# Optimization experiments

Hardware: AMD Instinct MI355X
Metric: run time of the kernel (lower is better)

The kernel has to match this reference:

```python
import jax, jax.numpy as jnp
import numpy as np

N = 50000
E = 800000
IN_DIM = 16
OUT_DIM = 16
EDGE_IN = 16
HID = 32


def setup_inputs() -> dict:
    key = jax.random.key(0)
    ks = jax.random.split(key, 9)
    x = jax.random.normal(ks[0], (N, IN_DIM), dtype=jnp.float32)
    edge_index = jax.random.randint(ks[1], (2, E), 0, N, dtype=jnp.int64)
    edge_attr = jax.random.normal(ks[2], (E, EDGE_IN), dtype=jnp.float32)
    # edge MLP params: Linear(EDGE_IN, 32) -> ReLU -> Linear(32, IN*OUT)
    w1 = jax.random.normal(ks[3], (EDGE_IN, HID), dtype=jnp.float32) * (1.0 / np.sqrt(EDGE_IN))
    b1 = jnp.zeros((HID,), dtype=jnp.float32)
    w2 = jax.random.normal(ks[4], (HID, IN_DIM * OUT_DIM), dtype=jnp.float32) * (1.0 / np.sqrt(HID))
    b2 = jnp.zeros((IN_DIM * OUT_DIM,), dtype=jnp.float32)
    # NNConv root weight and bias (defaults root_weight=True, bias=True)
    root = jax.random.normal(ks[5], (IN_DIM, OUT_DIM), dtype=jnp.float32) * (1.0 / np.sqrt(IN_DIM))
    bias = jnp.zeros((OUT_DIM,), dtype=jnp.float32)
    return {"x": x, "edge_index": edge_index, "edge_attr": edge_attr,
            "w1": w1, "b1": b1, "w2": w2, "b2": b2, "root": root, "bias": bias}


def reference(x, edge_index, edge_attr, w1, b1, w2, b2, root, bias):
    src = edge_index[0]  # x_j gathered from source nodes
    dst = edge_index[1]  # scatter-mean into target nodes
    # edge MLP -> per-edge weight matrix [E, IN, OUT]
    h = jax.nn.relu(edge_attr @ w1 + b1)
    W = (h @ w2 + b2).reshape(-1, IN_DIM, OUT_DIM)
    # per-edge matvec: message_e = x[src_e] @ W_e  -> [E, OUT]
    msg = jnp.einsum('ei,eio->eo', x[src], W)
    # scatter-mean aggregate into N target nodes
    summed = jax.ops.segment_sum(msg, dst, num_segments=N)
    cnt = jax.ops.segment_sum(jnp.ones((msg.shape[0],), dtype=msg.dtype), dst, num_segments=N)
    aggr = summed / jnp.maximum(cnt, 1.0)[:, None]
    return aggr + x @ root + bias
```

## Files before the change

kernel.cpp:

```cpp
#include <hip/hip_runtime.h>
#include <hip/hip_bf16.h>
#include <hip/hip_fp16.h>


#define N_NODES 50000
#define N_EDGES 800000
#define IN_D    16
#define OUT_D   16
#define HID_D   32
#define KTILES  17
#define NBLK_G  (N_NODES * OUT_D / 256)
#define EDGE_TPB   512
#define NBLK_E512  ((N_EDGES + EDGE_TPB - 1) / EDGE_TPB)
#define BLOB_BYTES 20480
#define BLOB_W1    17408
#define BLOB_B1    19456

typedef __attribute__((ext_vector_type(8))) _Float16 hfrag8;
typedef __attribute__((ext_vector_type(4))) float f32x4;

__device__ __forceinline__ void fma4(float a, const float4 w, float4& m) {
    m.x = fmaf(a, w.x, m.x);
    m.y = fmaf(a, w.y, m.y);
    m.z = fmaf(a, w.z, m.z);
    m.w = fmaf(a, w.w, m.w);
}
__device__ __forceinline__ int clampn(int v) {
    return v < 0 ? 0 : (v >= N_NODES ? N_NODES - 1 : v);
}
__device__ __forceinline__ void gload_lds16(const void* g, void* l) {
    __builtin_amdgcn_global_load_lds(
        (const __attribute__((address_space(1))) unsigned int*)g,
        (__attribute__((address_space(3))) unsigned int*)l,
        16, 0, 0);
}


__global__ __launch_bounds__(256) void setup_k(
    const float* __restrict__ w1,
    const float* __restrict__ b1,
    const float* __restrict__ w2,
    const float* __restrict__ b2,
    unsigned char* __restrict__ blob)
{
    const int t = threadIdx.x;
    __half* bp = reinterpret_cast<__half*>(blob);
    for (int r = t; r < KTILES * 32; r += 256) {
        const int tile = r >> 5, q = (r >> 3) & 3, j = r & 7;
        const int base = ((tile * 4 + q) * 16) * 8 + j;
        float vals[16];
        if (r < 512) {
            const float4* wr = reinterpret_cast<const float4*>(w2) + r * 4;
            float4 v0 = wr[0], v1 = wr[1], v2 = wr[2], v3 = wr[3];
            vals[0]=v0.x; vals[1]=v0.y; vals[2]=v0.z; vals[3]=v0.w;
            vals[4]=v1.x; vals[5]=v1.y; vals[6]=v1.z; vals[7]=v1.w;
            vals[8]=v2.x; vals[9]=v2.y; vals[10]=v2.z; vals[11]=v2.w;
            vals[12]=v3.x; vals[13]=v3.y; vals[14]=v3.z; vals[15]=v3.w;
        } else if (r < 528) {
            const float4* br = reinterpret_cast<const float4*>(b2) + (r - 512) * 4;
            float4 v0 = br[0], v1 = br[1], v2 = br[2], v3 = br[3];
            vals[0]=v0.x; vals[1]=v0.y; vals[2]=v0.z; vals[3]=v0.w;
            vals[4]=v1.x; vals[5]=v1.y; vals[6]=v1.z; vals[7]=v1.w;
            vals[8]=v2.x; vals[9]=v2.y; vals[10]=v2.z; vals[11]=v2.w;
            vals[12]=v3.x; vals[13]=v3.y; vals[14]=v3.z; vals[15]=v3.w;
        } else {
            #pragma unroll
            for (int o = 0; o < 16; ++o) vals[o] = 0.f;
        }
        #pragma unroll
        for (int o = 0; o < 16; ++o) bp[base + o * 8] = __float2half(vals[o]);
    }
    float* wf = reinterpret_cast<float*>(blob + BLOB_W1);
    wf[t] = w1[t];
    wf[t + 256] = w1[t + 256];
    if (t < HID_D) reinterpret_cast<float*>(blob + BLOB_B1)[t] = b1[t];
}


template <int MODE, int CAP>
__global__ __launch_bounds__(EDGE_TPB, 6) void edge_k(
    const float* __restrict__ x,
    const int*   __restrict__ ei,
    const float* __restrict__ ea,
    const unsigned char* __restrict__ gblob,
    int*   __restrict__ aux,
    int*   __restrict__ next,
    float* __restrict__ msg)
{
    __shared__ alignas(16) unsigned char s_blob[BLOB_BYTES];
    __shared__ alignas(16) __half s_h2[8 * 64 * 32];

    const int t    = threadIdx.x;
    const int lane = t & 63;
    const int w    = t >> 6;
    const int e    = blockIdx.x * EDGE_TPB + t;
    const bool wvalid = (blockIdx.x * EDGE_TPB + w * 64) < N_EDGES;

    #pragma unroll
    for (int j = 0; j < 3; ++j) {
        const int ch = w + 8 * j;
        if (ch < BLOB_BYTES / 1024)
            gload_lds16(gblob + ch * 1024 + lane * 16, s_blob + ch * 1024);
    }

    const hfrag8* s_B  = reinterpret_cast<const hfrag8*>(s_blob);
    const float4* s_w1 = reinterpret_cast<const float4*>(s_blob + BLOB_W1);
    const float4* s_b1 = reinterpret_cast<const float4*>(s_blob + BLOB_B1);

    const int q   = lane >> 4;
    const int n   = lane & 15;
    const int qh  = q >> 1;
    const int i0q = (q & 1) * 8;

    int slot = 0;
    float4 xpre[4][2];
    float eav[IN_D];

    if (wvalid) {
        const int src = clampn(ei[e]);
        const int dst = clampn(ei[N_EDGES + e]);
        if (MODE == 0) {
            int rank = atomicAdd(&aux[dst], 1);
            rank = rank < CAP ? rank : CAP - 1;
            slot = dst * CAP + rank;
        } else {
            next[e] = atomicExch(&aux[dst * 4 + (e & 3)], e);
            slot = e;
        }
        #pragma unroll
        for (int sub = 0; sub < 4; ++sub) {
            const int srcB = __shfl(src, sub * 16 + n, 64);
            const float4* xp = reinterpret_cast<const float4*>(x) + (size_t)srcB * 4 + (i0q >> 2);
            xpre[sub][0] = xp[0];
            xpre[sub][1] = xp[1];
        }
        const float4* eap = reinterpret_cast<const float4*>(ea) + (size_t)e * 4;
        float4 a0 = eap[0], a1 = eap[1], a2 = eap[2], a3 = eap[3];
        eav[0]=a0.x;  eav[1]=a0.y;  eav[2]=a0.z;  eav[3]=a0.w;
        eav[4]=a1.x;  eav[5]=a1.y;  eav[6]=a1.z;  eav[7]=a1.w;
        eav[8]=a2.x;  eav[9]=a2.y;  eav[10]=a2.z; eav[11]=a2.w;
        eav[12]=a3.x; eav[13]=a3.y; eav[14]=a3.z; eav[15]=a3.w;
    }

    __syncthreads();
    if (!wvalid) return;

    {
        float4 hv[HID_D / 4];
        #pragma unroll
        for (int j = 0; j < HID_D / 4; ++j) hv[j] = s_b1[j];
        #pragma unroll
        for (int i = 0; i < IN_D; ++i) {
            const float xi = eav[i];
            #pragma unroll
            for (int j = 0; j < HID_D / 4; ++j) fma4(xi, s_w1[i * (HID_D / 4) + j], hv[j]);
        }
        union { hfrag8 v[4]; __half h[32]; } hp;
        #pragma unroll
        for (int jj = 0; jj < 8; ++jj) {
            const int k0 = 4 * jj;
            hp.h[((k0 + 0) & 1) * 16 + ((k0 + 0) >> 1)] = __float2half(fmaxf(hv[jj].x, 0.f));
            hp.h[((k0 + 1) & 1) * 16 + ((k0 + 1) >> 1)] = __float2half(fmaxf(hv[jj].y, 0.f));
            hp.h[((k0 + 2) & 1) * 16 + ((k0 + 2) >> 1)] = __float2half(fmaxf(hv[jj].z, 0.f));
            hp.h[((k0 + 3) & 1) * 16 + ((k0 + 3) >> 1)] = __float2half(fmaxf(hv[jj].w, 0.f));
        }
        hfrag8* rowv = reinterpret_cast<hfrag8*>(s_h2 + (size_t)w * 2048 + lane * 32);
        const int swl = (lane >> 1) & 3;
        rowv[0 ^ swl] = hp.v[0];
        rowv[1 ^ swl] = hp.v[1];
        rowv[2 ^ swl] = hp.v[2];
        rowv[3 ^ swl] = hp.v[3];
    }
    asm volatile("s_waitcnt lgkmcnt(0)" ::: "memory");
    __builtin_amdgcn_wave_barrier();

    const __half* hbase = s_h2 + (size_t)w * 2048;
    #pragma unroll
    for (int sub = 0; sub < 4; ++sub) {
        const int posW = sub * 16 + n;
        __half2 xh[4];
        {
            float4 xa = xpre[sub][0], xb = xpre[sub][1];
            xh[0] = __float22half2_rn(make_float2(xa.x, xa.y));
            xh[1] = __float22half2_rn(make_float2(xa.z, xa.w));
            xh[2] = __float22half2_rn(make_float2(xb.x, xb.y));
            xh[3] = __float22half2_rn(make_float2(xb.z, xb.w));
        }
        union { hfrag8 v; __half h[8]; } hA, hB;
        {
            const hfrag8* rowv = reinterpret_cast<const hfrag8*>(hbase + posW * 32);
            const int swr = (posW >> 1) & 3;
            hA.v = rowv[(2 * qh + 0) ^ swr];
            hB.v = rowv[(2 * qh + 1) ^ swr];
        }
        f32x4 acc = {0.f, 0.f, 0.f, 0.f};
        #pragma unroll
        for (int tile = 0; tile < 16; ++tile) {
            const __half hs = (tile < 8) ? hA.h[tile] : hB.h[tile - 8];
            const __half2 hh = __half2half2(hs);
            union { hfrag8 v; __half2 h[4]; } a;
            a.h[0] = __hmul2(hh, xh[0]);
            a.h[1] = __hmul2(hh, xh[1]);
            a.h[2] = __hmul2(hh, xh[2]);
            a.h[3] = __hmul2(hh, xh[3]);
            acc = __builtin_amdgcn_mfma_f32_16x16x32_f16(a.v, s_B[tile * 64 + lane], acc, 0, 0, 0);
        }
        {
            union { hfrag8 v; __half2 h[4]; } a;
            if (qh == 0) { a.h[0]=xh[0]; a.h[1]=xh[1]; a.h[2]=xh[2]; a.h[3]=xh[3]; }
            else { hfrag8 z = {0,0,0,0,0,0,0,0}; a.v = z; }
            acc = __builtin_amdgcn_mfma_f32_16x16x32_f16(a.v, s_B[16 * 64 + lane], acc, 0, 0, 0);
        }
        #pragma unroll
        for (int r = 0; r < 4; ++r) {
            const int slotB = __shfl(slot, sub * 16 + q * 4 + r, 64);
            msg[(size_t)slotB * 16 + n] = acc[r];
        }
    }
}


template <int CAP>
__global__ __launch_bounds__(256) void gather_cap(
    const float* __restrict__ x,
    const float* __restrict__ root,
    const float* __restrict__ bias,
    const float* __restrict__ msg,
    const int*   __restrict__ cnt,
    float* __restrict__ out)
{
    __shared__ float4 s_root4[IN_D * 4];
    __shared__ float4 s_bias4[4];
    const int t = threadIdx.x;
    if (t < IN_D * 4) s_root4[t] = reinterpret_cast<const float4*>(root)[t];
    if (t < 4)        s_bias4[t] = reinterpret_cast<const float4*>(bias)[t];
    __syncthreads();

    const int g = blockIdx.x * 256 + t;
    const int n = g >> 4;
    const int l = t & 15;
    const int c = l >> 2;
    const int p = l & 3;

    const int d = cnt[n];
    const int m = d < CAP ? d : CAP;

    const float4* base = reinterpret_cast<const float4*>(msg) + (size_t)n * CAP * 4 + p;
    float4 a0 = make_float4(0.f, 0.f, 0.f, 0.f);
    float4 a1 = make_float4(0.f, 0.f, 0.f, 0.f);
    int j = c;
    for (; j + 4 < m; j += 8) {
        float4 v0 = base[(size_t)j * 4];
        float4 v1 = base[(size_t)(j + 4) * 4];
        a0.x += v0.x; a0.y += v0.y; a0.z += v0.z; a0.w += v0.w;
        a1.x += v1.x; a1.y += v1.y; a1.z += v1.z; a1.w += v1.w;
    }
    if (j < m) {
        float4 v0 = base[(size_t)j * 4];
        a0.x += v0.x; a0.y += v0.y; a0.z += v0.z; a0.w += v0.w;
    }
    float4 acc = make_float4(a0.x + a1.x, a0.y + a1.y, a0.z + a1.z, a0.w + a1.w);

    acc.x += __shfl_xor(acc.x, 4); acc.y += __shfl_xor(acc.y, 4);
    acc.z += __shfl_xor(acc.z, 4); acc.w += __shfl_xor(acc.w, 4);
    acc.x += __shfl_xor(acc.x, 8); acc.y += __shfl_xor(acc.y, 8);
    acc.z += __shfl_xor(acc.z, 8); acc.w += __shfl_xor(acc.w, 8);

    const float inv = 1.0f / (float)(d > 1 ? d : 1);
    float4 mv = s_bias4[p];
    mv.x += acc.x * inv; mv.y += acc.y * inv; mv.z += acc.z * inv; mv.w += acc.w * inv;

    {
        const float4* xp = reinterpret_cast<const float4*>(x) + (size_t)n * 4;
        float4 x0 = xp[0], x1 = xp[1], x2 = xp[2], x3 = xp[3];
        const float xs[IN_D] = { x0.x,x0.y,x0.z,x0.w, x1.x,x1.y,x1.z,x1.w,
                                 x2.x,x2.y,x2.z,x2.w, x3.x,x3.y,x3.z,x3.w };
        #pragma unroll
        for (int i = 0; i < IN_D; ++i) fma4(xs[i], s_root4[i * 4 + p], mv);
    }

    if (c == 0)
        reinterpret_cast<float4*>(out + (size_t)n * 16)[p] = mv;
}


__global__ __launch_bounds__(256) void gather_ll4(
    const float* __restrict__ x,
    const float* __restrict__ root,
    const float* __restrict__ bias,
    const float* __restrict__ msg,
    const int*   __restrict__ head4,
    const int*   __restrict__ next,
    float* __restrict__ out)
{
    __shared__ float4 s_root4[IN_D * 4];
    __shared__ float4 s_bias4[4];
    const int t = threadIdx.x;
    if (t < IN_D * 4) s_root4[t] = reinterpret_cast<const float4*>(root)[t];
    if (t < 4)        s_bias4[t] = reinterpret_cast<const float4*>(bias)[t];
    __syncthreads();

    const int g = blockIdx.x * 256 + t;
    const int n = g >> 4;
    const int l = t & 15;
    const int c = l >> 2;
    const int p = l & 3;

    float4 acc = make_float4(0.f, 0.f, 0.f, 0.f);
    int cnt = 0;
    int j = head4[n * 4 + c];
    while (j >= 0) {
        const float4 v = reinterpret_cast<const float4*>(msg + (size_t)j * 16)[p];
        acc.x += v.x; acc.y += v.y; acc.z += v.z; acc.w += v.w;
        ++cnt;
        j = next[j];
    }

    acc.x += __shfl_xor(acc.x, 4); acc.y += __shfl_xor(acc.y, 4);
    acc.z += __shfl_xor(acc.z, 4); acc.w += __shfl_xor(acc.w, 4);
    cnt   += __shfl_xor(cnt, 4);
    acc.x += __shfl_xor(acc.x, 8); acc.y += __shfl_xor(acc.y, 8);
    acc.z += __shfl_xor(acc.z, 8); acc.w += __shfl_xor(acc.w, 8);
    cnt   += __shfl_xor(cnt, 8);

    const float inv = 1.0f / (float)(cnt > 1 ? cnt : 1);
    float4 m = s_bias4[p];
    m.x += acc.x * inv; m.y += acc.y * inv; m.z += acc.z * inv; m.w += acc.w * inv;

    {
        const float4* xp = reinterpret_cast<const float4*>(x) + (size_t)n * 4;
        float4 x0 = xp[0], x1 = xp[1], x2 = xp[2], x3 = xp[3];
        const float xs[IN_D] = { x0.x,x0.y,x0.z,x0.w, x1.x,x1.y,x1.z,x1.w,
                                 x2.x,x2.y,x2.z,x2.w, x3.x,x3.y,x3.z,x3.w };
        #pragma unroll
        for (int i = 0; i < IN_D; ++i) fma4(xs[i], s_root4[i * 4 + p], m);
    }

    if (c == 0)
        reinterpret_cast<float4*>(out + (size_t)n * 16)[p] = m;
}

extern "C" void kernel_launch(void* const* d_in, const int* in_sizes, int n_in,
                              void* d_out, int out_size, void* d_ws, size_t ws_size,
                              hipStream_t stream) {
    const float* x    = (const float*)d_in[0];
    const int*   ei   = (const int*)  d_in[1];
    const float* ea   = (const float*)d_in[2];
    const float* w1   = (const float*)d_in[3];
    const float* b1   = (const float*)d_in[4];
    const float* w2   = (const float*)d_in[5];
    const float* b2   = (const float*)d_in[6];
    const float* root = (const float*)d_in[7];
    const float* bias = (const float*)d_in[8];
    float* out = (float*)d_out;

    unsigned char* blob = (unsigned char*)d_ws;

    const size_t need64 = (size_t)BLOB_BYTES + (size_t)N_NODES * 4 + (size_t)N_NODES * 64 * 64;
    const size_t need48 = (size_t)BLOB_BYTES + (size_t)N_NODES * 4 + (size_t)N_NODES * 48 * 64;

    setup_k<<<1, 256, 0, stream>>>(w1, b1, w2, b2, blob);

    if (ws_size >= need64) {
        int*   cnt = (int*)(blob + BLOB_BYTES);
        float* msg = (float*)(blob + BLOB_BYTES + (size_t)N_NODES * 4);
        hipMemsetAsync(cnt, 0, N_NODES * sizeof(int), stream);
        edge_k<0, 64><<<NBLK_E512, EDGE_TPB, 0, stream>>>(x, ei, ea, blob, cnt, nullptr, msg);
        gather_cap<64><<<NBLK_G, 256, 0, stream>>>(x, root, bias, msg, cnt, out);
    } else if (ws_size >= need48) {
        int*   cnt = (int*)(blob + BLOB_BYTES);
        float* msg = (float*)(blob + BLOB_BYTES + (size_t)N_NODES * 4);
        hipMemsetAsync(cnt, 0, N_NODES * sizeof(int), stream);
        edge_k<0, 48><<<NBLK_E512, EDGE_TPB, 0, stream>>>(x, ei, ea, blob, cnt, nullptr, msg);
        gather_cap<48><<<NBLK_G, 256, 0, stream>>>(x, root, bias, msg, cnt, out);
    } else {
        int*   head4 = (int*)(blob + BLOB_BYTES);
        int*   next  = head4 + N_NODES * 4;
        float* msg   = (float*)(next + N_EDGES);
        edge_k<1, 0><<<NBLK_E512, EDGE_TPB, 0, stream>>>(x, ei, ea, blob, head4, next, msg);
        gather_ll4  <<<NBLK_G, 256, 0, stream>>>(x, root, bias, msg, head4, next, out);
    }
}
```

Baseline: 195.2 us.

## Replace capped per-node message slots with CSR layout built by degree count and scan

Adds a degree-counting pass fused into the setup kernel, a single-block prefix scan that builds CSR offsets, and has the edge kernel write messages into compact CSR slots via an atomic cursor. The gather then reads contiguous per-node message ranges instead of a fixed CAP-strided buffer. This shrinks the message buffer, improves gather locality and removes the degree cap. The cost is an extra counting pass over the edge indices and a serial one-block scan. The edge kernel also drops from 512 to 256 threads per block.

Result: slower. 327.2 us (+67.6%).

```diff
diff --git a/kernel.cpp b/kernel.cpp
--- a/kernel.cpp
+++ b/kernel.cpp
@@ -9,12 +9,17 @@
 #define OUT_D   16
 #define HID_D   32
 #define KTILES  17
+#define NBLK_E  (N_EDGES / 256)
 #define NBLK_G  (N_NODES * OUT_D / 256)
-#define EDGE_TPB   512
-#define NBLK_E512  ((N_EDGES + EDGE_TPB - 1) / EDGE_TPB)
 #define BLOB_BYTES 20480
 #define BLOB_W1    17408
 #define BLOB_B1    19456
+
+#define WS_DEG  20480
+#define WS_OFF  220480
+#define WS_CUR  420544
+#define WS_MSG  620544
+#define WS_NEED (620544 + (size_t)N_EDGES * 16 * 4)
 
 typedef __attribute__((ext_vector_type(8))) _Float16 hfrag8;
 typedef __attribute__((ext_vector_type(4))) float f32x4;
@@ -36,14 +41,21 @@
 }
 
 
-__global__ __launch_bounds__(256) void setup_k(
+__global__ __launch_bounds__(256) void setup_count_k(
     const float* __restrict__ w1,
     const float* __restrict__ b1,
     const float* __restrict__ w2,
     const float* __restrict__ b2,
-    unsigned char* __restrict__ blob)
+    const int*   __restrict__ ei,
+    unsigned char* __restrict__ blob,
+    int* __restrict__ deg)
 {
     const int t = threadIdx.x;
+    if (blockIdx.x != 0) {
+        const int e = (blockIdx.x - 1) * 256 + t;
+        atomicAdd(&deg[clampn(ei[N_EDGES + e])], 1);
+        return;
+    }
     __half* bp = reinterpret_cast<__half*>(blob);
     for (int r = t; r < KTILES * 32; r += 256) {
         const int tile = r >> 5, q = (r >> 3) & 3, j = r & 7;
@@ -71,14 +83,51 @@
         for (int o = 0; o < 16; ++o) bp[base + o * 8] = __float2half(vals[o]);
     }
     float* wf = reinterpret_cast<float*>(blob + BLOB_W1);
-    wf[t] = w1[t];
+    wf[t]       = w1[t];
     wf[t + 256] = w1[t + 256];
     if (t < HID_D) reinterpret_cast<float*>(blob + BLOB_B1)[t] = b1[t];
 }
 
 
-template <int MODE, int CAP>
-__global__ __launch_bounds__(EDGE_TPB, 6) void edge_k(
+__global__ __launch_bounds__(1024) void scan_k(
+    const int* __restrict__ deg,
+    int* __restrict__ off,
+    int* __restrict__ cur)
+{
+    __shared__ int s[1024];
+    const int t = threadIdx.x;
+    const int CH = 49;
+    const int base = t * CH;
+
+    int tot = 0;
+    for (int i = 0; i < CH; ++i) {
+        const int n = base + i;
+        if (n < N_NODES) tot += deg[n];
+    }
+    s[t] = tot;
+    __syncthreads();
+    for (int d = 1; d < 1024; d <<= 1) {
+        const int v   = s[t];
+        const int add = (t >= d) ? s[t - d] : 0;
+        __syncthreads();
+        s[t] = v + add;
+        __syncthreads();
+    }
+    int run = (t == 0) ? 0 : s[t - 1];
+    for (int i = 0; i < CH; ++i) {
+        const int n = base + i;
+        if (n < N_NODES) {
+            off[n] = run;
+            cur[n] = run;
+            run += deg[n];
+        }
+    }
+    if (t == 1023) off[N_NODES] = run;
+}
+
+
+template <int MODE>
+__global__ __launch_bounds__(256) void edge_k(
     const float* __restrict__ x,
     const int*   __restrict__ ei,
     const float* __restrict__ ea,
@@ -88,19 +137,17 @@
     float* __restrict__ msg)
 {
     __shared__ alignas(16) unsigned char s_blob[BLOB_BYTES];
-    __shared__ alignas(16) __half s_h2[8 * 64 * 32];
+    __shared__ alignas(16) __half s_h2[4 * 64 * 32];
 
     const int t    = threadIdx.x;
     const int lane = t & 63;
     const int w    = t >> 6;
-    const int e    = blockIdx.x * EDGE_TPB + t;
-    const bool wvalid = (blockIdx.x * EDGE_TPB + w * 64) < N_EDGES;
+    const int e    = blockIdx.x * 256 + t;
 
     #pragma unroll
-    for (int j = 0; j < 3; ++j) {
-        const int ch = w + 8 * j;
-        if (ch < BLOB_BYTES / 1024)
-            gload_lds16(gblob + ch * 1024 + lane * 16, s_blob + ch * 1024);
+    for (int j = 0; j < 5; ++j) {
+        const int ch = w + 4 * j;
+        gload_lds16(gblob + ch * 1024 + lane * 16, s_blob + ch * 1024);
     }
 
     const hfrag8* s_B  = reinterpret_cast<const hfrag8*>(s_blob);
@@ -112,28 +159,25 @@
     const int qh  = q >> 1;
     const int i0q = (q & 1) * 8;
 
-    int slot = 0;
+    const int src = clampn(ei[e]);
+    const int dst = clampn(ei[N_EDGES + e]);
+    int slot;
+    if (MODE == 0) {
+        slot = atomicAdd(&aux[dst], 1);
+    } else {
+        next[e] = atomicExch(&aux[dst * 4 + (e & 3)], e);
+        slot = e;
+    }
     float4 xpre[4][2];
+    #pragma unroll
+    for (int sub = 0; sub < 4; ++sub) {
+        const int srcB = __shfl(src, sub * 16 + n, 64);
+        const float4* xp = reinterpret_cast<const float4*>(x) + (size_t)srcB * 4 + (i0q >> 2);
+        xpre[sub][0] = xp[0];
+        xpre[sub][1] = xp[1];
+    }
     float eav[IN_D];
-
-    if (wvalid) {
-        const int src = clampn(ei[e]);
-        const int dst = clampn(ei[N_EDGES + e]);
-        if (MODE == 0) {
-            int rank = atomicAdd(&aux[dst], 1);
-            rank = rank < CAP ? rank : CAP - 1;
-            slot = dst * CAP + rank;
-        } else {
-            next[e] = atomicExch(&aux[dst * 4 + (e & 3)], e);
-            slot = e;
-        }
-        #pragma unroll
-        for (int sub = 0; sub < 4; ++sub) {
-            const int srcB = __shfl(src, sub * 16 + n, 64);
-            const float4* xp = reinterpret_cast<const float4*>(x) + (size_t)srcB * 4 + (i0q >> 2);
-            xpre[sub][0] = xp[0];
-            xpre[sub][1] = xp[1];
-        }
+    {
         const float4* eap = reinterpret_cast<const float4*>(ea) + (size_t)e * 4;
         float4 a0 = eap[0], a1 = eap[1], a2 = eap[2], a3 = eap[3];
         eav[0]=a0.x;  eav[1]=a0.y;  eav[2]=a0.z;  eav[3]=a0.w;
@@ -143,7 +187,6 @@
     }
 
     __syncthreads();
-    if (!wvalid) return;
 
     {
         float4 hv[HID_D / 4];
@@ -220,13 +263,12 @@
 }
 
 
-template <int CAP>
-__global__ __launch_bounds__(256) void gather_cap(
+__global__ __launch_bounds__(256) void gather_csr(
     const float* __restrict__ x,
     const float* __restrict__ root,
     const float* __restrict__ bias,
     const float* __restrict__ msg,
-    const int*   __restrict__ cnt,
+    const int*   __restrict__ off,
     float* __restrict__ out)
 {
     __shared__ float4 s_root4[IN_D * 4];
@@ -242,20 +284,20 @@
     const int c = l >> 2;
     const int p = l & 3;
 
-    const int d = cnt[n];
-    const int m = d < CAP ? d : CAP;
-
-    const float4* base = reinterpret_cast<const float4*>(msg) + (size_t)n * CAP * 4 + p;
+    const int s0 = off[n];
+    const int d  = off[n + 1] - s0;
+
+    const float4* base = reinterpret_cast<const float4*>(msg) + (size_t)s0 * 4 + p;
     float4 a0 = make_float4(0.f, 0.f, 0.f, 0.f);
     float4 a1 = make_float4(0.f, 0.f, 0.f, 0.f);
     int j = c;
-    for (; j + 4 < m; j += 8) {
+    for (; j + 4 < d; j += 8) {
         float4 v0 = base[(size_t)j * 4];
         float4 v1 = base[(size_t)(j + 4) * 4];
         a0.x += v0.x; a0.y += v0.y; a0.z += v0.z; a0.w += v0.w;
         a1.x += v1.x; a1.y += v1.y; a1.z += v1.z; a1.w += v1.w;
     }
-    if (j < m) {
+    if (j < d) {
         float4 v0 = base[(size_t)j * 4];
         a0.x += v0.x; a0.y += v0.y; a0.z += v0.z; a0.w += v0.w;
     }
@@ -354,30 +396,25 @@
     const float* bias = (const float*)d_in[8];
     float* out = (float*)d_out;
 
-    unsigned char* blob = (unsigned char*)d_ws;
-
-    const size_t need64 = (size_t)BLOB_BYTES + (size_t)N_NODES * 4 + (size_t)N_NODES * 64 * 64;
-    const size_t need48 = (size_t)BLOB_BYTES + (size_t)N_NODES * 4 + (size_t)N_NODES * 48 * 64;
-
-    setup_k<<<1, 256, 0, stream>>>(w1, b1, w2, b2, blob);
-
-    if (ws_size >= need64) {
-        int*   cnt = (int*)(blob + BLOB_BYTES);
-        float* msg = (float*)(blob + BLOB_BYTES + (size_t)N_NODES * 4);
-        hipMemsetAsync(cnt, 0, N_NODES * sizeof(int), stream);
-        edge_k<0, 64><<<NBLK_E512, EDGE_TPB, 0, stream>>>(x, ei, ea, blob, cnt, nullptr, msg);
-        gather_cap<64><<<NBLK_G, 256, 0, stream>>>(x, root, bias, msg, cnt, out);
-    } else if (ws_size >= need48) {
-        int*   cnt = (int*)(blob + BLOB_BYTES);
-        float* msg = (float*)(blob + BLOB_BYTES + (size_t)N_NODES * 4);
-        hipMemsetAsync(cnt, 0, N_NODES * sizeof(int), stream);
-        edge_k<0, 48><<<NBLK_E512, EDGE_TPB, 0, stream>>>(x, ei, ea, blob, cnt, nullptr, msg);
-        gather_cap<48><<<NBLK_G, 256, 0, stream>>>(x, root, bias, msg, cnt, out);
+    unsigned char* ws = (unsigned char*)d_ws;
+    unsigned char* blob = ws;
+
+    if (ws_size >= WS_NEED) {
+        int*   deg = (int*)(ws + WS_DEG);
+        int*   off = (int*)(ws + WS_OFF);
+        int*   cur = (int*)(ws + WS_CUR);
+        float* msg = (float*)(ws + WS_MSG);
+        hipMemsetAsync(deg, 0, N_NODES * sizeof(int), stream);
+        setup_count_k<<<NBLK_E + 1, 256, 0, stream>>>(w1, b1, w2, b2, ei, blob, deg);
+        scan_k<<<1, 1024, 0, stream>>>(deg, off, cur);
+        edge_k<0><<<NBLK_E, 256, 0, stream>>>(x, ei, ea, blob, cur, nullptr, msg);
+        gather_csr<<<NBLK_G, 256, 0, stream>>>(x, root, bias, msg, off, out);
     } else {
-        int*   head4 = (int*)(blob + BLOB_BYTES);
+        int*   head4 = (int*)(ws + BLOB_BYTES);
         int*   next  = head4 + N_NODES * 4;
         float* msg   = (float*)(next + N_EDGES);
-        edge_k<1, 0><<<NBLK_E512, EDGE_TPB, 0, stream>>>(x, ei, ea, blob, head4, next, msg);
+        setup_count_k<<<1, 256, 0, stream>>>(w1, b1, w2, b2, ei, blob, (int*)(ws + BLOB_BYTES));
+        edge_k<1><<<NBLK_E, 256, 0, stream>>>(x, ei, ea, blob, head4, next, msg);
         gather_ll4  <<<NBLK_G, 256, 0, stream>>>(x, root, bias, msg, head4, next, out);
     }
 }
```

## Replace per-slot message buffer with direct float atomic scatter into node sums

Applied to the files above, without the earlier changes.

The edge kernel now adds each edge message straight into a per-node sum buffer with hardware float atomics and counts degree with an integer atomic. This removes the capped per-destination message slots or linked lists and the gather pass that read them back. The node kernel becomes a simple per-element normalize plus root matmul. Block size drops to 256 threads. The cost is 16 float atomics per edge, which raises contention on the destination rows and makes the summation order nondeterministic.

Result: faster. 184.3 us (-5.6%).

```diff
diff --git a/kernel.cpp b/kernel.cpp
--- a/kernel.cpp
+++ b/kernel.cpp
@@ -9,12 +9,15 @@
 #define OUT_D   16
 #define HID_D   32
 #define KTILES  17
-#define NBLK_G  (N_NODES * OUT_D / 256)
-#define EDGE_TPB   512
-#define NBLK_E512  ((N_EDGES + EDGE_TPB - 1) / EDGE_TPB)
+#define NBLK_E  (N_EDGES / 256)
+#define NBLK_N  (N_NODES * OUT_D / 256)
 #define BLOB_BYTES 20480
 #define BLOB_W1    17408
 #define BLOB_B1    19456
+
+#define WS_SUM   20480
+#define WS_DEG   3220480
+#define WS_NEED  (3220480 + (size_t)N_NODES * 4)
 
 typedef __attribute__((ext_vector_type(8))) _Float16 hfrag8;
 typedef __attribute__((ext_vector_type(4))) float f32x4;
@@ -71,36 +74,32 @@
         for (int o = 0; o < 16; ++o) bp[base + o * 8] = __float2half(vals[o]);
     }
     float* wf = reinterpret_cast<float*>(blob + BLOB_W1);
-    wf[t] = w1[t];
+    wf[t]       = w1[t];
     wf[t + 256] = w1[t + 256];
     if (t < HID_D) reinterpret_cast<float*>(blob + BLOB_B1)[t] = b1[t];
 }
 
 
-template <int MODE, int CAP>
-__global__ __launch_bounds__(EDGE_TPB, 6) void edge_k(
+__global__ __launch_bounds__(256) void edge_k(
     const float* __restrict__ x,
     const int*   __restrict__ ei,
     const float* __restrict__ ea,
     const unsigned char* __restrict__ gblob,
-    int*   __restrict__ aux,
-    int*   __restrict__ next,
-    float* __restrict__ msg)
+    int*   __restrict__ deg,
+    float* __restrict__ sum)
 {
     __shared__ alignas(16) unsigned char s_blob[BLOB_BYTES];
-    __shared__ alignas(16) __half s_h2[8 * 64 * 32];
+    __shared__ alignas(16) __half s_h2[4 * 64 * 32];
 
     const int t    = threadIdx.x;
     const int lane = t & 63;
     const int w    = t >> 6;
-    const int e    = blockIdx.x * EDGE_TPB + t;
-    const bool wvalid = (blockIdx.x * EDGE_TPB + w * 64) < N_EDGES;
-
-    #pragma unroll
-    for (int j = 0; j < 3; ++j) {
-        const int ch = w + 8 * j;
-        if (ch < BLOB_BYTES / 1024)
-            gload_lds16(gblob + ch * 1024 + lane * 16, s_blob + ch * 1024);
+    const int e    = blockIdx.x * 256 + t;
+
+    #pragma unroll
+    for (int j = 0; j < 5; ++j) {
+        const int ch = w + 4 * j;
+        gload_lds16(gblob + ch * 1024 + lane * 16, s_blob + ch * 1024);
     }
 
     const hfrag8* s_B  = reinterpret_cast<const hfrag8*>(s_blob);
@@ -112,28 +111,20 @@
     const int qh  = q >> 1;
     const int i0q = (q & 1) * 8;
 
-    int slot = 0;
+    const int src = clampn(ei[e]);
+    const int dst = clampn(ei[N_EDGES + e]);
+    atomicAdd(&deg[dst], 1);
+
     float4 xpre[4][2];
+    #pragma unroll
+    for (int sub = 0; sub < 4; ++sub) {
+        const int srcB = __shfl(src, sub * 16 + n, 64);
+        const float4* xp = reinterpret_cast<const float4*>(x) + (size_t)srcB * 4 + (i0q >> 2);
+        xpre[sub][0] = xp[0];
+        xpre[sub][1] = xp[1];
+    }
     float eav[IN_D];
-
-    if (wvalid) {
-        const int src = clampn(ei[e]);
-        const int dst = clampn(ei[N_EDGES + e]);
-        if (MODE == 0) {
-            int rank = atomicAdd(&aux[dst], 1);
-            rank = rank < CAP ? rank : CAP - 1;
-            slot = dst * CAP + rank;
-        } else {
-            next[e] = atomicExch(&aux[dst * 4 + (e & 3)], e);
-            slot = e;
-        }
-        #pragma unroll
-        for (int sub = 0; sub < 4; ++sub) {
-            const int srcB = __shfl(src, sub * 16 + n, 64);
-            const float4* xp = reinterpret_cast<const float4*>(x) + (size_t)srcB * 4 + (i0q >> 2);
-            xpre[sub][0] = xp[0];
-            xpre[sub][1] = xp[1];
-        }
+    {
         const float4* eap = reinterpret_cast<const float4*>(ea) + (size_t)e * 4;
         float4 a0 = eap[0], a1 = eap[1], a2 = eap[2], a3 = eap[3];
         eav[0]=a0.x;  eav[1]=a0.y;  eav[2]=a0.z;  eav[3]=a0.w;
@@ -143,7 +134,6 @@
     }
 
     __syncthreads();
-    if (!wvalid) return;
 
     {
         float4 hv[HID_D / 4];
@@ -213,131 +203,50 @@
         }
         #pragma unroll
         for (int r = 0; r < 4; ++r) {
-            const int slotB = __shfl(slot, sub * 16 + q * 4 + r, 64);
-            msg[(size_t)slotB * 16 + n] = acc[r];
-        }
-    }
-}
-
-
-template <int CAP>
-__global__ __launch_bounds__(256) void gather_cap(
+            const int dstB = __shfl(dst, sub * 16 + q * 4 + r, 64);
+            unsafeAtomicAdd(&sum[(size_t)dstB * 16 + n], acc[r]);
+        }
+    }
+}
+
+
+__global__ __launch_bounds__(256) void node_k(
     const float* __restrict__ x,
     const float* __restrict__ root,
     const float* __restrict__ bias,
-    const float* __restrict__ msg,
-    const int*   __restrict__ cnt,
+    const float* __restrict__ sum,
+    const int*   __restrict__ deg,
     float* __restrict__ out)
 {
-    __shared__ float4 s_root4[IN_D * 4];
-    __shared__ float4 s_bias4[4];
+    __shared__ float s_root[IN_D * OUT_D];
+    __shared__ float s_bias[OUT_D];
     const int t = threadIdx.x;
-    if (t < IN_D * 4) s_root4[t] = reinterpret_cast<const float4*>(root)[t];
-    if (t < 4)        s_bias4[t] = reinterpret_cast<const float4*>(bias)[t];
+    s_root[t] = root[t];
+    if (t < OUT_D) s_bias[t] = bias[t];
     __syncthreads();
 
     const int g = blockIdx.x * 256 + t;
     const int n = g >> 4;
-    const int l = t & 15;
-    const int c = l >> 2;
-    const int p = l & 3;
-
-    const int d = cnt[n];
-    const int m = d < CAP ? d : CAP;
-
-    const float4* base = reinterpret_cast<const float4*>(msg) + (size_t)n * CAP * 4 + p;
-    float4 a0 = make_float4(0.f, 0.f, 0.f, 0.f);
-    float4 a1 = make_float4(0.f, 0.f, 0.f, 0.f);
-    int j = c;
-    for (; j + 4 < m; j += 8) {
-        float4 v0 = base[(size_t)j * 4];
-        float4 v1 = base[(size_t)(j + 4) * 4];
-        a0.x += v0.x; a0.y += v0.y; a0.z += v0.z; a0.w += v0.w;
-        a1.x += v1.x; a1.y += v1.y; a1.z += v1.z; a1.w += v1.w;
-    }
-    if (j < m) {
-        float4 v0 = base[(size_t)j * 4];
-        a0.x += v0.x; a0.y += v0.y; a0.z += v0.z; a0.w += v0.w;
-    }
-    float4 acc = make_float4(a0.x + a1.x, a0.y + a1.y, a0.z + a1.z, a0.w + a1.w);
-
-    acc.x += __shfl_xor(acc.x, 4); acc.y += __shfl_xor(acc.y, 4);
-    acc.z += __shfl_xor(acc.z, 4); acc.w += __shfl_xor(acc.w, 4);
-    acc.x += __shfl_xor(acc.x, 8); acc.y += __shfl_xor(acc.y, 8);
-    acc.z += __shfl_xor(acc.z, 8); acc.w += __shfl_xor(acc.w, 8);
-
-    const float inv = 1.0f / (float)(d > 1 ? d : 1);
-    float4 mv = s_bias4[p];
-    mv.x += acc.x * inv; mv.y += acc.y * inv; mv.z += acc.z * inv; mv.w += acc.w * inv;
-
+    const int o = g & 15;
+
+    const float s = sum[g];
+    const int   d = deg[n];
+    float mv = s * (1.0f / (float)(d > 1 ? d : 1)) + s_bias[o];
+
+    float xs[IN_D];
     {
         const float4* xp = reinterpret_cast<const float4*>(x) + (size_t)n * 4;
-        float4 x0 = xp[0], x1 = xp[1], x2 = xp[2], x3 = xp[3];
-        const float xs[IN_D] = { x0.x,x0.y,x0.z,x0.w, x1.x,x1.y,x1.z,x1.w,
-                                 x2.x,x2.y,x2.z,x2.w, x3.x,x3.y,x3.z,x3.w };
-        #pragma unroll
-        for (int i = 0; i < IN_D; ++i) fma4(xs[i], s_root4[i * 4 + p], mv);
-    }
-
-    if (c == 0)
-        reinterpret_cast<float4*>(out + (size_t)n * 16)[p] = mv;
-}
-
-
-__global__ __launch_bounds__(256) void gather_ll4(
-    const float* __restrict__ x,
-    const float* __restrict__ root,
-    const float* __restrict__ bias,
-    const float* __restrict__ msg,
-    const int*   __restrict__ head4,
-    const int*   __restrict__ next,
-    float* __restrict__ out)
-{
-    __shared__ float4 s_root4[IN_D * 4];
-    __shared__ float4 s_bias4[4];
-    const int t = threadIdx.x;
-    if (t < IN_D * 4) s_root4[t] = reinterpret_cast<const float4*>(root)[t];
-    if (t < 4)        s_bias4[t] = reinterpret_cast<const float4*>(bias)[t];
-    __syncthreads();
-
-    const int g = blockIdx.x * 256 + t;
-    const int n = g >> 4;
-    const int l = t & 15;
-    const int c = l >> 2;
-    const int p = l & 3;
-
-    float4 acc = make_float4(0.f, 0.f, 0.f, 0.f);
-    int cnt = 0;
-    int j = head4[n * 4 + c];
-    while (j >= 0) {
-        const float4 v = reinterpret_cast<const float4*>(msg + (size_t)j * 16)[p];
-        acc.x += v.x; acc.y += v.y; acc.z += v.z; acc.w += v.w;
-        ++cnt;
-        j = next[j];
-    }
-
-    acc.x += __shfl_xor(acc.x, 4); acc.y += __shfl_xor(acc.y, 4);
-    acc.z += __shfl_xor(acc.z, 4); acc.w += __shfl_xor(acc.w, 4);
-    cnt   += __shfl_xor(cnt, 4);
-    acc.x += __shfl_xor(acc.x, 8); acc.y += __shfl_xor(acc.y, 8);
-    acc.z += __shfl_xor(acc.z, 8); acc.w += __shfl_xor(acc.w, 8);
-    cnt   += __shfl_xor(cnt, 8);
-
-    const float inv = 1.0f / (float)(cnt > 1 ? cnt : 1);
-    float4 m = s_bias4[p];
-    m.x += acc.x * inv; m.y += acc.y * inv; m.z += acc.z * inv; m.w += acc.w * inv;
-
-    {
-        const float4* xp = reinterpret_cast<const float4*>(x) + (size_t)n * 4;
-        float4 x0 = xp[0], x1 = xp[1], x2 = xp[2], x3 = xp[3];
-        const float xs[IN_D] = { x0.x,x0.y,x0.z,x0.w, x1.x,x1.y,x1.z,x1.w,
-                                 x2.x,x2.y,x2.z,x2.w, x3.x,x3.y,x3.z,x3.w };
-        #pragma unroll
-        for (int i = 0; i < IN_D; ++i) fma4(xs[i], s_root4[i * 4 + p], m);
-    }
-
-    if (c == 0)
-        reinterpret_cast<float4*>(out + (size_t)n * 16)[p] = m;
+        float4 b0 = xp[0], b1v = xp[1], b2v = xp[2], b3 = xp[3];
+        xs[0]=b0.x;  xs[1]=b0.y;  xs[2]=b0.z;  xs[3]=b0.w;
+        xs[4]=b1v.x; xs[5]=b1v.y; xs[6]=b1v.z; xs[7]=b1v.w;
+        xs[8]=b2v.x; xs[9]=b2v.y; xs[10]=b2v.z; xs[11]=b2v.w;
+        xs[12]=b3.x; xs[13]=b3.y; xs[14]=b3.z; xs[15]=b3.w;
+    }
+    #pragma unroll
+    for (int i = 0; i < IN_D; ++i)
+        mv = fmaf(xs[i], s_root[i * OUT_D + o], mv);
+
+    out[g] = mv;
 }
 
 extern "C" void kernel_launch(void* const* d_in, const int* in_sizes, int n_in,
@@ -354,30 +263,13 @@
     const float* bias = (const float*)d_in[8];
     float* out = (float*)d_out;
 
-    unsigned char* blob = (unsigned char*)d_ws;
-
-    const size_t need64 = (size_t)BLOB_BYTES + (size_t)N_NODES * 4 + (size_t)N_NODES * 64 * 64;
-    const size_t need48 = (size_t)BLOB_BYTES + (size_t)N_NODES * 4 + (size_t)N_NODES * 48 * 64;
-
+    unsigned char* ws   = (unsigned char*)d_ws;
+    unsigned char* blob = ws;
+    float* sum = (float*)(ws + WS_SUM);
+    int*   deg = (int*)(ws + WS_DEG);
+
+    hipMemsetAsync(ws + WS_SUM, 0, (size_t)N_NODES * 16 * 4 + (size_t)N_NODES * 4, stream);
     setup_k<<<1, 256, 0, stream>>>(w1, b1, w2, b2, blob);
-
-    if (ws_size >= need64) {
-        int*   cnt = (int*)(blob + BLOB_BYTES);
-        float* msg = (float*)(blob + BLOB_BYTES + (size_t)N_NODES * 4);
-        hipMemsetAsync(cnt, 0, N_NODES * sizeof(int), stream);
-        edge_k<0, 64><<<NBLK_E512, EDGE_TPB, 0, stream>>>(x, ei, ea, blob, cnt, nullptr, msg);
-        gather_cap<64><<<NBLK_G, 256, 0, stream>>>(x, root, bias, msg, cnt, out);
-    } else if (ws_size >= need48) {
-        int*   cnt = (int*)(blob + BLOB_BYTES);
-        float* msg = (float*)(blob + BLOB_BYTES + (size_t)N_NODES * 4);
-        hipMemsetAsync(cnt, 0, N_NODES * sizeof(int), stream);
-        edge_k<0, 48><<<NBLK_E512, EDGE_TPB, 0, stream>>>(x, ei, ea, blob, cnt, nullptr, msg);
-        gather_cap<48><<<NBLK_G, 256, 0, stream>>>(x, root, bias, msg, cnt, out);
-    } else {
-        int*   head4 = (int*)(blob + BLOB_BYTES);
-        int*   next  = head4 + N_NODES * 4;
-        float* msg   = (float*)(next + N_EDGES);
-        edge_k<1, 0><<<NBLK_E512, EDGE_TPB, 0, stream>>>(x, ei, ea, blob, head4, next, msg);
-        gather_ll4  <<<NBLK_G, 256, 0, stream>>>(x, root, bias, msg, head4, next, out);
-    }
-}
+    edge_k<<<NBLK_E, 256, 0, stream>>>(x, ei, ea, blob, deg, sum);
+    node_k<<<NBLK_N, 256, 0, stream>>>(x, root, bias, sum, deg, out);
+}
```
